# Kernel tuning notes

Hardware: AMD Instinct MI355X
Metric: run time of the kernel (lower is better)

Reference implementation:

```python
import jax, jax.numpy as jnp
import numpy as np

# AdaptiveLogSoftmaxWithLoss config (input_dim=2048, n_classes=50257, div_value=4.0)
CUTOFFS = [1000, 10000, 50257]  # torch appends n_classes
N_CLUSTERS = 2                   # len(CUTOFFS) - 1
HEAD_SIZE = CUTOFFS[0] + N_CLUSTERS  # 1002
D = 2048
HSZ = [D // 4, D // 16]          # tail hidden sizes: [512, 128]
N_TOK = 4096


def setup_inputs() -> dict:
    key = jax.random.key(0)
    ks = jax.random.split(key, 7)
    w = 0.02  # weight scale so logits stay O(1)
    x = jax.random.normal(ks[0], (N_TOK, D), dtype=jnp.float32)
    W_head = jax.random.normal(ks[1], (HEAD_SIZE, D), dtype=jnp.float32) * w
    W1_0 = jax.random.normal(ks[2], (HSZ[0], D), dtype=jnp.float32) * w
    W2_0 = jax.random.normal(ks[3], (CUTOFFS[1] - CUTOFFS[0], HSZ[0]), dtype=jnp.float32) * w  # [9000, 512]
    W1_1 = jax.random.normal(ks[4], (HSZ[1], D), dtype=jnp.float32) * w
    W2_1 = jax.random.normal(ks[5], (CUTOFFS[2] - CUTOFFS[1], HSZ[1]), dtype=jnp.float32) * w  # [40257, 128]
    target = jax.random.randint(ks[6], (N_TOK,), 0, CUTOFFS[2], dtype=jnp.int32)
    return {"x": x, "target": target, "W_head": W_head,
            "W1_0": W1_0, "W2_0": W2_0, "W1_1": W1_1, "W2_1": W2_1}


def reference(x, target, W_head, W1_0, W2_0, W1_1, W2_1):
    # head: [N, 1002] = [1000 frequent classes | 2 cluster logits]
    head = x @ W_head.T
    head_lsm = jax.nn.log_softmax(head, axis=-1)

    t = target
    # log-prob of target if it lies in the head (clip keeps gather in-range; masked later)
    head_lp = jnp.take_along_axis(head_lsm, jnp.clip(t, 0, CUTOFFS[0] - 1)[:, None], axis=1)[:, 0]

    def tail_target_lp(W1, W2, low, high, cluster_idx):
        # two-stage projection: [N,D] @ [D,h] @ [h,osz]
        logits = (x @ W1.T) @ W2.T                     # [N, high-low]
        lsm = jax.nn.log_softmax(logits, axis=-1)
        idx = jnp.clip(t - low, 0, high - low - 1)
        g = jnp.take_along_axis(lsm, idx[:, None], axis=1)[:, 0]
        # combine with head's cluster log-prob
        return head_lsm[:, CUTOFFS[0] + cluster_idx] + g

    lp0 = tail_target_lp(W1_0, W2_0, CUTOFFS[0], CUTOFFS[1], 0)
    lp1 = tail_target_lp(W1_1, W2_1, CUTOFFS[1], CUTOFFS[2], 1)

    out = jnp.where(t < CUTOFFS[0], head_lp, jnp.where(t < CUTOFFS[1], lp0, lp1))
    loss = -jnp.mean(out)
    return out, loss
```

## Files before the change

### kernel.cpp

```cpp
#include <hip/hip_runtime.h>
#include <hip/hip_bf16.h>
#include <math.h>

#define NTOK 4096
#define DIM 2048
#define NHEAD 1002
#define NCAT 1664
#define C0LO 1000
#define C0HI 10000
#define OSZ0 9000
#define OSZ1 40257
#define H0S 512
#define H1S 128
#define JS0 24
#define JS1 16
#define HEADBLKS 8
#define NT0 71
#define NT1 315

typedef __attribute__((ext_vector_type(4))) short short4v;
typedef __attribute__((ext_vector_type(8))) short short8v;
typedef __attribute__((ext_vector_type(4))) float f32x4;
typedef __hip_bfloat16 bf16;

#define GLOBAL_AS __attribute__((address_space(1)))
#define LDS_AS __attribute__((address_space(3)))

#define RAW_BAR() __builtin_amdgcn_s_barrier()
#define SCHED_FENCE() __builtin_amdgcn_sched_barrier(0)
#define WAIT_VM(N) asm volatile("s_waitcnt vmcnt(" #N ")" ::: "memory")
#define WAIT_LGKM0() asm volatile("s_waitcnt lgkmcnt(0)" ::: "memory")

__global__ __launch_bounds__(256) void cvt_all(
    const float* __restrict__ x, const float* __restrict__ W_head,
    const float* __restrict__ W1_0, const float* __restrict__ W1_1,
    const float* __restrict__ W2_0, const float* __restrict__ W2_1,
    bf16* __restrict__ xb, bf16* __restrict__ Wcat,
    bf16* __restrict__ W20b, bf16* __restrict__ W21b) {
  const long NX = (long)NTOK * DIM / 8;
  const long NC = (long)NCAT * DIM / 8;
  const long N20 = (long)OSZ0 * H0S / 8;
  const long N21 = (long)OSZ1 * H1S / 8;
  long gid = (long)blockIdx.x * 256 + threadIdx.x;
  const float* src = nullptr;
  bf16* dst;
  if (gid < NX) {
    src = x + gid * 8; dst = xb + gid * 8;
  } else if (gid < NX + NC) {
    long o = (gid - NX) * 8;
    int row = (int)(o >> 11), k = (int)(o & 2047);
    dst = Wcat + o;
    if (row < NHEAD) src = W_head + (long)row * DIM + k;
    else if (row < 1024) src = nullptr;
    else if (row < 1536) src = W1_0 + (long)(row - 1024) * DIM + k;
    else src = W1_1 + (long)(row - 1536) * DIM + k;
  } else if (gid < NX + NC + N20) {
    long o = (gid - NX - NC) * 8; src = W2_0 + o; dst = W20b + o;
  } else if (gid < NX + NC + N20 + N21) {
    long o = (gid - NX - NC - N20) * 8; src = W2_1 + o; dst = W21b + o;
  } else {
    return;
  }
  union { short8v v; bf16 h[8]; } u;
  if (src) {
    float4 a = *reinterpret_cast<const float4*>(src);
    float4 b = *reinterpret_cast<const float4*>(src + 4);
    u.h[0] = __float2bfloat16(a.x); u.h[1] = __float2bfloat16(a.y);
    u.h[2] = __float2bfloat16(a.z); u.h[3] = __float2bfloat16(a.w);
    u.h[4] = __float2bfloat16(b.x); u.h[5] = __float2bfloat16(b.y);
    u.h[6] = __float2bfloat16(b.z); u.h[7] = __float2bfloat16(b.w);
  } else {
#pragma unroll
    for (int e = 0; e < 8; ++e) u.h[e] = __float2bfloat16(0.f);
  }
  *reinterpret_cast<short8v*>(dst) = u.v;
}

__device__ __forceinline__ void stage_tile(const bf16* __restrict__ g, int row0,
                                           int maxrow, int ld, int k0,
                                           char* lds, int wave, int lane) {
#pragma unroll
  for (int c = 0; c < 4; ++c) {
    int rbase = wave * 32 + c * 8;
    int row = rbase + (lane >> 3);
    int grow = row0 + row;
    grow = grow < maxrow ? grow : maxrow;
    int slot = (lane & 7) ^ (row & 7);
    const bf16* src = g + (size_t)grow * ld + k0 + slot * 8;
    __builtin_amdgcn_global_load_lds((const GLOBAL_AS unsigned int*)src,
                                     (LDS_AS unsigned int*)(lds + rbase * 128),
                                     16, 0, 0);
  }
}

__device__ __forceinline__ short8v read_frag(const char* lds, int row, int kk, int lane) {
  int g = lane >> 4;
  int r7 = row & 7;
  int b1 = kk * 64 + g * 8;
  int b2 = b1 + 32;
  b1 = ((b1 >> 4) ^ r7) * 16 + (b1 & 15);
  b2 = ((b2 >> 4) ^ r7) * 16 + (b2 & 15);
  const char* p = lds + row * 128;
  short4v lo = *reinterpret_cast<const short4v*>(p + b1);
  short4v hi = *reinterpret_cast<const short4v*>(p + b2);
  return __builtin_shufflevector(lo, hi, 0, 1, 2, 3, 4, 5, 6, 7);
}

__device__ __forceinline__ void stage_tile256(const bf16* __restrict__ g, int row0,
                                              int maxrow, int ld,
                                              char* lds, int wave, int lane) {
#pragma unroll
  for (int c = 0; c < 8; ++c) {
    int rbase = wave * 32 + c * 4;
    int row = rbase + (lane >> 4);
    int grow = row0 + row;
    grow = grow < maxrow ? grow : maxrow;
    int slot = (lane & 15) ^ (row & 7);
    const bf16* src = g + (size_t)grow * ld + slot * 8;
    __builtin_amdgcn_global_load_lds((const GLOBAL_AS unsigned int*)src,
                                     (LDS_AS unsigned int*)(lds + rbase * 256),
                                     16, 0, 0);
  }
}

__device__ __forceinline__ short8v read_frag256(const char* lds, int row, int kk, int lane) {
  int g = lane >> 4;
  int r7 = row & 7;
  int b1 = kk * 64 + g * 8;
  int b2 = b1 + 32;
  b1 = (((b1 >> 4) ^ r7) << 4) | (b1 & 15);
  b2 = (((b2 >> 4) ^ r7) << 4) | (b2 & 15);
  const char* p = lds + row * 256;
  short4v lo = *reinterpret_cast<const short4v*>(p + b1);
  short4v hi = *reinterpret_cast<const short4v*>(p + b2);
  return __builtin_shufflevector(lo, hi, 0, 1, 2, 3, 4, 5, 6, 7);
}

__device__ __forceinline__ void reduce_write_ps(float srun[4][4], float* reds,
                                                float* ps, int slice, int tok0,
                                                int lane, int wr, int wc) {
#pragma unroll
  for (int off = 1; off < 16; off <<= 1)
#pragma unroll
    for (int m = 0; m < 4; ++m)
#pragma unroll
      for (int r = 0; r < 4; ++r) srun[m][r] += __shfl_xor(srun[m][r], off);
  __syncthreads();
  if (wc == 0 && (lane & 15) == 0) {
#pragma unroll
    for (int m = 0; m < 4; ++m)
#pragma unroll
      for (int r = 0; r < 4; ++r)
        reds[wr * 64 + m * 16 + (lane >> 4) * 4 + r] = srun[m][r];
  }
  __syncthreads();
  if (wc == 1 && (lane & 15) == 0) {
#pragma unroll
    for (int m = 0; m < 4; ++m)
#pragma unroll
      for (int r = 0; r < 4; ++r) {
        int row = wr * 64 + m * 16 + (lane >> 4) * 4 + r;
        ps[(size_t)slice * NTOK + tok0 + row] = reds[row] + srun[m][r];
      }
  }
}

__global__ __launch_bounds__(256, 3) void tail0_lse(
    const bf16* __restrict__ Ab, const bf16* __restrict__ W2b,
    float* __restrict__ ps) {
  __shared__ __align__(16) char As[128 * 128];
  __shared__ __align__(16) char Bs[128 * 128];
  __shared__ float reds[128];
  int tid = threadIdx.x;
  int lane = tid & 63, wave = tid >> 6;
  int wr = wave >> 1, wc = wave & 1;
  int wgid = blockIdx.x;
  int cx = wgid & 7, w = wgid >> 3;
  int tb = cx * 4 + (w & 3);
  int ys = w >> 2;
  int tok0 = tb * 128;
  int t_lo = (NT0 * ys) / JS0, t_hi = (NT0 * (ys + 1)) / JS0;
  float srun[4][4] = {};
  for (int jt = t_lo; jt < t_hi; ++jt) {
    int j0 = jt * 128;
    f32x4 acc[4][4] = {};
    for (int k0 = 0; k0 < H0S; k0 += 64) {
      __syncthreads();
      stage_tile(Ab, tok0, NTOK - 1, H0S, k0, As, wave, lane);
      stage_tile(W2b, j0, OSZ0 - 1, H0S, k0, Bs, wave, lane);
      __syncthreads();
#pragma unroll
      for (int kk = 0; kk < 2; ++kk) {
        short8v af[4], bfr[4];
#pragma unroll
        for (int m = 0; m < 4; ++m)
          af[m] = read_frag(As, wr * 64 + m * 16 + (lane & 15), kk, lane);
#pragma unroll
        for (int n = 0; n < 4; ++n)
          bfr[n] = read_frag(Bs, wc * 64 + n * 16 + (lane & 15), kk, lane);
#pragma unroll
        for (int m = 0; m < 4; ++m)
#pragma unroll
          for (int n = 0; n < 4; ++n)
            acc[m][n] = __builtin_amdgcn_mfma_f32_16x16x32_bf16(af[m], bfr[n], acc[m][n], 0, 0, 0);
      }
    }
#pragma unroll
    for (int m = 0; m < 4; ++m)
#pragma unroll
      for (int n = 0; n < 4; ++n) {
        int col = j0 + wc * 64 + n * 16 + (lane & 15);
        if (col < OSZ0) {
#pragma unroll
          for (int r = 0; r < 4; ++r) srun[m][r] += __expf(acc[m][n][r]);
        }
      }
  }
  reduce_write_ps(srun, reds, ps, ys, tok0, lane, wr, wc);
}

__device__ void tail1_body(const bf16* __restrict__ Ab, const bf16* __restrict__ W2b,
                           float* __restrict__ ps, char* lds) {
  char* buf0 = lds;
  char* buf1 = lds + 32768;
  float* reds = (float*)(lds + 65536);
  int tid = threadIdx.x;
  int lane = tid & 63, wave = tid >> 6;
  int wr = wave >> 1, wc = wave & 1;
  int wgid = blockIdx.x;
  int cx = wgid & 7, w = wgid >> 3;
  int tb = cx * 4 + (w & 3);
  int ys = w >> 2;
  int tok0 = tb * 128;
  int t_lo = (NT1 * ys) / JS1, t_hi = (NT1 * (ys + 1)) / JS1;
  int nt = t_hi - t_lo;

  stage_tile256(Ab, tok0, NTOK - 1, H1S, buf1, wave, lane);
  WAIT_VM(0); SCHED_FENCE();
  RAW_BAR();
  short8v afr[4][4];
#pragma unroll
  for (int kk = 0; kk < 4; ++kk)
#pragma unroll
    for (int m = 0; m < 4; ++m)
      afr[kk][m] = read_frag256(buf1, wr * 64 + m * 16 + (lane & 15), kk, lane);
  stage_tile256(W2b, t_lo * 128, OSZ1 - 1, H1S, buf0, wave, lane);
  WAIT_LGKM0(); SCHED_FENCE();
  RAW_BAR();
  if (nt > 1) stage_tile256(W2b, (t_lo + 1) * 128, OSZ1 - 1, H1S, buf1, wave, lane);

  float srun[4][4] = {};
  for (int i = 0; i < nt; ++i) {
    char* cur = (i & 1) ? buf1 : buf0;
    if (i + 1 < nt) { WAIT_VM(8); } else { WAIT_VM(0); }
    SCHED_FENCE();
    RAW_BAR();
    int j0 = (t_lo + i) * 128;
    f32x4 acc[4][4] = {};
#pragma unroll
    for (int kk = 0; kk < 4; ++kk) {
      short8v bfr[4];
#pragma unroll
      for (int n = 0; n < 4; ++n)
        bfr[n] = read_frag256(cur, wc * 64 + n * 16 + (lane & 15), kk, lane);
#pragma unroll
      for (int m = 0; m < 4; ++m)
#pragma unroll
        for (int n = 0; n < 4; ++n)
          acc[m][n] = __builtin_amdgcn_mfma_f32_16x16x32_bf16(afr[kk][m], bfr[n], acc[m][n], 0, 0, 0);
    }
#pragma unroll
    for (int m = 0; m < 4; ++m)
#pragma unroll
      for (int n = 0; n < 4; ++n) {
        int col = j0 + wc * 64 + n * 16 + (lane & 15);
        if (col < OSZ1) {
#pragma unroll
          for (int r = 0; r < 4; ++r) srun[m][r] += __expf(acc[m][n][r]);
        }
      }
    SCHED_FENCE();
    RAW_BAR();
    if (i + 2 < nt) stage_tile256(W2b, (t_lo + i + 2) * 128, OSZ1 - 1, H1S, cur, wave, lane);
  }
  reduce_write_ps(srun, reds, ps, ys, tok0, lane, wr, wc);
}

__global__ __launch_bounds__(256, 2) void tail1_lse(
    const bf16* __restrict__ Ab, const bf16* __restrict__ W2b,
    float* __restrict__ ps) {
  __shared__ __align__(16) char lds[66048];
  tail1_body(Ab, W2b, ps, lds);
}

__global__ __launch_bounds__(256, 3) void proj_gemm(
    const bf16* __restrict__ A, const bf16* __restrict__ B,
    float* __restrict__ head, float* __restrict__ h0, bf16* __restrict__ h0b,
    float* __restrict__ h1, bf16* __restrict__ h1b, float* __restrict__ ps_head) {
  __shared__ __align__(16) char As[16384];
  __shared__ __align__(16) char Bs[16384];
  __shared__ float reds[128];
  int tid = threadIdx.x;
  int lane = tid & 63, wave = tid >> 6;
  int wr = wave >> 1, wc = wave & 1;
  int wgid = blockIdx.x;
  int cx = wgid & 7, w = wgid >> 3;
  int col_b = w >> 2;
  int row_b = cx * 4 + (w & 3);
  int row0 = row_b * 128, col0 = col_b * 128;
  f32x4 acc[4][4] = {};
  for (int k0 = 0; k0 < DIM; k0 += 64) {
    __syncthreads();
    stage_tile(A, row0, NTOK - 1, DIM, k0, As, wave, lane);
    stage_tile(B, col0, NCAT - 1, DIM, k0, Bs, wave, lane);
    __syncthreads();
#pragma unroll
    for (int kk = 0; kk < 2; ++kk) {
      short8v af[4], bfr[4];
#pragma unroll
      for (int m = 0; m < 4; ++m)
        af[m] = read_frag(As, wr * 64 + m * 16 + (lane & 15), kk, lane);
#pragma unroll
      for (int n = 0; n < 4; ++n)
        bfr[n] = read_frag(Bs, wc * 64 + n * 16 + (lane & 15), kk, lane);
#pragma unroll
      for (int m = 0; m < 4; ++m)
#pragma unroll
        for (int n = 0; n < 4; ++n)
          acc[m][n] = __builtin_amdgcn_mfma_f32_16x16x32_bf16(af[m], bfr[n], acc[m][n], 0, 0, 0);
    }
  }
  float srun[4][4] = {};
#pragma unroll
  for (int m = 0; m < 4; ++m) {
    int row = row0 + wr * 64 + m * 16 + (lane >> 4) * 4;
#pragma unroll
    for (int n = 0; n < 4; ++n) {
      int col = col0 + wc * 64 + n * 16 + (lane & 15);
#pragma unroll
      for (int r = 0; r < 4; ++r) {
        float v = acc[m][n][r];
        if (col < NHEAD) {
          head[(size_t)(row + r) * NHEAD + col] = v;
          srun[m][r] += __expf(v);
        } else if (col >= 1024 && col < 1536) {
          h0[(size_t)(row + r) * H0S + (col - 1024)] = v;
          h0b[(size_t)(row + r) * H0S + (col - 1024)] = __float2bfloat16(v);
        } else if (col >= 1536) {
          h1[(size_t)(row + r) * H1S + (col - 1536)] = v;
          h1b[(size_t)(row + r) * H1S + (col - 1536)] = __float2bfloat16(v);
        }
      }
    }
  }
  if (col_b < HEADBLKS) {
    reduce_write_ps(srun, reds, ps_head, col_b, row0, lane, wr, wc);
  }
}

__global__ __launch_bounds__(256) void finalize2(
    const int* __restrict__ target, const float* __restrict__ head,
    const float* __restrict__ ps_head,
    const float* __restrict__ h0, const float* __restrict__ h1,
    const float* __restrict__ W2_0, const float* __restrict__ W2_1,
    const float* __restrict__ ps0, const float* __restrict__ ps1,
    float* __restrict__ out) {
  int warp = threadIdx.x >> 6, lane = threadIdx.x & 63;
  int i = blockIdx.x * 4 + warp;
  if (i >= NTOK) return;
  int t = target[i];
  float sh = 0.f;
#pragma unroll
  for (int s = 0; s < HEADBLKS; ++s) sh += ps_head[(size_t)s * NTOK + i];
  float lse_head = logf(sh);
  float res;
  if (t < C0LO) {
    res = head[(size_t)i * NHEAD + t] - lse_head;
  } else {
    int c = (t < C0HI) ? 0 : 1;
    int H = c ? H1S : H0S;
    int low = c ? C0HI : C0LO;
    const float* hv = (c ? h1 : h0) + (size_t)i * H;
    const float* wv = (c ? W2_1 : W2_0) + (size_t)(t - low) * H;
    float p = 0.f;
    for (int k = lane * 4; k < H; k += 256) {
      float4 a = *reinterpret_cast<const float4*>(hv + k);
      float4 b = *reinterpret_cast<const float4*>(wv + k);
      p += a.x * b.x + a.y * b.y + a.z * b.z + a.w * b.w;
    }
#pragma unroll
    for (int off = 32; off > 0; off >>= 1) p += __shfl_xor(p, off);
    const float* ps = c ? ps1 : ps0;
    int js = c ? JS1 : JS0;
    float S = 0.f;
    for (int s = 0; s < js; ++s) S += ps[(size_t)s * NTOK + i];
    float cl = head[(size_t)i * NHEAD + C0LO + c];
    res = (cl - lse_head) + (p - logf(S));
  }
  if (lane == 0) out[i] = res;
}

__global__ __launch_bounds__(256) void loss_kernel(float* __restrict__ out) {
  __shared__ float red[256];
  int tid = threadIdx.x;
  float s = 0.f;
  for (int j = tid; j < NTOK; j += 256) s += out[j];
  red[tid] = s; __syncthreads();
  for (int off = 128; off > 0; off >>= 1) {
    if (tid < off) red[tid] += red[tid + off];
    __syncthreads();
  }
  if (tid == 0) out[NTOK] = -red[0] / (float)NTOK;
}

extern "C" void kernel_launch(void* const* d_in, const int* in_sizes, int n_in,
                              void* d_out, int out_size, void* d_ws, size_t ws_size,
                              hipStream_t stream) {
  (void)in_sizes; (void)n_in; (void)out_size; (void)ws_size;
  const float* x = (const float*)d_in[0];
  const int* target = (const int*)d_in[1];
  const float* W_head = (const float*)d_in[2];
  const float* W1_0 = (const float*)d_in[3];
  const float* W2_0 = (const float*)d_in[4];
  const float* W1_1 = (const float*)d_in[5];
  const float* W2_1 = (const float*)d_in[6];
  float* out = (float*)d_out;

  char* w = (char*)d_ws;
  size_t off = 0;
  auto alloc = [&](size_t bytes) -> void* {
    void* p = w + off;
    off = (off + bytes + 255) & ~(size_t)255;
    return p;
  };
  bf16* xb   = (bf16*)alloc((size_t)NTOK * DIM * 2);
  bf16* Wcat = (bf16*)alloc((size_t)NCAT * DIM * 2);
  bf16* W20b = (bf16*)alloc((size_t)OSZ0 * H0S * 2);
  bf16* W21b = (bf16*)alloc((size_t)OSZ1 * H1S * 2);
  float* head = (float*)alloc((size_t)NTOK * NHEAD * 4);
  float* h0   = (float*)alloc((size_t)NTOK * H0S * 4);
  bf16*  h0b  = (bf16*)alloc((size_t)NTOK * H0S * 2);
  float* h1   = (float*)alloc((size_t)NTOK * H1S * 4);
  bf16*  h1b  = (bf16*)alloc((size_t)NTOK * H1S * 2);
  float* ps_head = (float*)alloc((size_t)HEADBLKS * NTOK * 4);
  float* ps0 = (float*)alloc((size_t)JS0 * NTOK * 4);
  float* ps1 = (float*)alloc((size_t)JS1 * NTOK * 4);

  dim3 blk(256);
  const long TOT8 = (long)NTOK * DIM / 8 + (long)NCAT * DIM / 8 +
                    (long)OSZ0 * H0S / 8 + (long)OSZ1 * H1S / 8;
  cvt_all<<<dim3((unsigned)((TOT8 + 255) / 256)), blk, 0, stream>>>(
      x, W_head, W1_0, W1_1, W2_0, W2_1, xb, Wcat, W20b, W21b);

  proj_gemm<<<dim3(416), blk, 0, stream>>>(
      xb, Wcat, head, h0, h0b, h1, h1b, ps_head);

  tail0_lse<<<dim3(32 * JS0), blk, 0, stream>>>(h0b, W20b, ps0);
  tail1_lse<<<dim3(32 * JS1), blk, 0, stream>>>(h1b, W21b, ps1);

  finalize2<<<dim3(NTOK / 4), blk, 0, stream>>>(target, head, ps_head, h0, h1,
                                                W2_0, W2_1, ps0, ps1, out);
  loss_kernel<<<1, blk, 0, stream>>>(out);
}
```

Measured before the change: 208.3 us.

## Pre-permute bf16 K layout so MFMA fragments load as single 16-byte LDS reads

The conversion kernel and the proj_gemm epilogue now write bf16 operands with the K dimension permuted in groups of 32. Each MFMA fragment therefore sits in one contiguous 16-byte chunk, and read_frag becomes a single 128-bit LDS load instead of two 64-bit loads plus a shuffle. Because the permutation is applied to both operands, the dot products are unchanged. The tail kernels also switch from a swizzled 1D block-index mapping to a plain 2D grid, which drops the earlier L2-locality block ordering.

```diff
diff --git a/kernel.cpp b/kernel.cpp
--- a/kernel.cpp
+++ b/kernel.cpp
@@ -31,6 +31,10 @@
 #define WAIT_VM(N) asm volatile("s_waitcnt vmcnt(" #N ")" ::: "memory")
 #define WAIT_LGKM0() asm volatile("s_waitcnt lgkmcnt(0)" ::: "memory")
 
+__device__ __forceinline__ int kperm(int c) {
+  return (c & ~31) | (((c & 15) >> 2) << 3) | (((c >> 4) & 1) << 2) | (c & 3);
+}
+
 __global__ __launch_bounds__(256) void cvt_all(
     const float* __restrict__ x, const float* __restrict__ W_head,
     const float* __restrict__ W1_0, const float* __restrict__ W1_1,
@@ -42,29 +46,44 @@
   const long N20 = (long)OSZ0 * H0S / 8;
   const long N21 = (long)OSZ1 * H1S / 8;
   long gid = (long)blockIdx.x * 256 + threadIdx.x;
-  const float* src = nullptr;
+  const float* s1 = nullptr;
+  const float* s2 = nullptr;
   bf16* dst;
+  long rel;
   if (gid < NX) {
-    src = x + gid * 8; dst = xb + gid * 8;
+    rel = gid * 8;
+    long c1 = (rel & ~31L) + ((rel >> 3) & 3) * 4;
+    s1 = x + c1; s2 = x + c1 + 16;
+    dst = xb + rel;
   } else if (gid < NX + NC) {
-    long o = (gid - NX) * 8;
-    int row = (int)(o >> 11), k = (int)(o & 2047);
-    dst = Wcat + o;
-    if (row < NHEAD) src = W_head + (long)row * DIM + k;
-    else if (row < 1024) src = nullptr;
-    else if (row < 1536) src = W1_0 + (long)(row - 1024) * DIM + k;
-    else src = W1_1 + (long)(row - 1536) * DIM + k;
+    rel = (gid - NX) * 8;
+    int row = (int)(rel >> 11);
+    long c1 = (rel & ~31L) + ((rel >> 3) & 3) * 4;
+    int col = (int)(c1 & 2047);
+    dst = Wcat + rel;
+    const float* srow = nullptr;
+    if (row < NHEAD) srow = W_head + (long)row * DIM;
+    else if (row < 1024) srow = nullptr;
+    else if (row < 1536) srow = W1_0 + (long)(row - 1024) * DIM;
+    else srow = W1_1 + (long)(row - 1536) * DIM;
+    if (srow) { s1 = srow + col; s2 = srow + col + 16; }
   } else if (gid < NX + NC + N20) {
-    long o = (gid - NX - NC) * 8; src = W2_0 + o; dst = W20b + o;
+    rel = (gid - NX - NC) * 8;
+    long c1 = (rel & ~31L) + ((rel >> 3) & 3) * 4;
+    s1 = W2_0 + c1; s2 = W2_0 + c1 + 16;
+    dst = W20b + rel;
   } else if (gid < NX + NC + N20 + N21) {
-    long o = (gid - NX - NC - N20) * 8; src = W2_1 + o; dst = W21b + o;
+    rel = (gid - NX - NC - N20) * 8;
+    long c1 = (rel & ~31L) + ((rel >> 3) & 3) * 4;
+    s1 = W2_1 + c1; s2 = W2_1 + c1 + 16;
+    dst = W21b + rel;
   } else {
     return;
   }
   union { short8v v; bf16 h[8]; } u;
-  if (src) {
-    float4 a = *reinterpret_cast<const float4*>(src);
-    float4 b = *reinterpret_cast<const float4*>(src + 4);
+  if (s1) {
+    float4 a = *reinterpret_cast<const float4*>(s1);
+    float4 b = *reinterpret_cast<const float4*>(s2);
     u.h[0] = __float2bfloat16(a.x); u.h[1] = __float2bfloat16(a.y);
     u.h[2] = __float2bfloat16(a.z); u.h[3] = __float2bfloat16(a.w);
     u.h[4] = __float2bfloat16(b.x); u.h[5] = __float2bfloat16(b.y);
@@ -94,16 +113,8 @@
 }
 
 __device__ __forceinline__ short8v read_frag(const char* lds, int row, int kk, int lane) {
-  int g = lane >> 4;
-  int r7 = row & 7;
-  int b1 = kk * 64 + g * 8;
-  int b2 = b1 + 32;
-  b1 = ((b1 >> 4) ^ r7) * 16 + (b1 & 15);
-  b2 = ((b2 >> 4) ^ r7) * 16 + (b2 & 15);
-  const char* p = lds + row * 128;
-  short4v lo = *reinterpret_cast<const short4v*>(p + b1);
-  short4v hi = *reinterpret_cast<const short4v*>(p + b2);
-  return __builtin_shufflevector(lo, hi, 0, 1, 2, 3, 4, 5, 6, 7);
+  int slot = (kk * 4 + (lane >> 4)) ^ (row & 7);
+  return *reinterpret_cast<const short8v*>(lds + row * 128 + slot * 16);
 }
 
 __device__ __forceinline__ void stage_tile256(const bf16* __restrict__ g, int row0,
@@ -124,16 +135,8 @@
 }
 
 __device__ __forceinline__ short8v read_frag256(const char* lds, int row, int kk, int lane) {
-  int g = lane >> 4;
-  int r7 = row & 7;
-  int b1 = kk * 64 + g * 8;
-  int b2 = b1 + 32;
-  b1 = (((b1 >> 4) ^ r7) << 4) | (b1 & 15);
-  b2 = (((b2 >> 4) ^ r7) << 4) | (b2 & 15);
-  const char* p = lds + row * 256;
-  short4v lo = *reinterpret_cast<const short4v*>(p + b1);
-  short4v hi = *reinterpret_cast<const short4v*>(p + b2);
-  return __builtin_shufflevector(lo, hi, 0, 1, 2, 3, 4, 5, 6, 7);
+  int slot = (kk * 4 + (lane >> 4)) ^ (row & 7);
+  return *reinterpret_cast<const short8v*>(lds + row * 256 + slot * 16);
 }
 
 __device__ __forceinline__ void reduce_write_ps(float srun[4][4], float* reds,
@@ -174,11 +177,8 @@
   int tid = threadIdx.x;
   int lane = tid & 63, wave = tid >> 6;
   int wr = wave >> 1, wc = wave & 1;
-  int wgid = blockIdx.x;
-  int cx = wgid & 7, w = wgid >> 3;
-  int tb = cx * 4 + (w & 3);
-  int ys = w >> 2;
-  int tok0 = tb * 128;
+  int tok0 = blockIdx.x * 128;
+  int ys = blockIdx.y;
   int t_lo = (NT0 * ys) / JS0, t_hi = (NT0 * (ys + 1)) / JS0;
   float srun[4][4] = {};
   for (int jt = t_lo; jt < t_hi; ++jt) {
@@ -227,11 +227,8 @@
   int tid = threadIdx.x;
   int lane = tid & 63, wave = tid >> 6;
   int wr = wave >> 1, wc = wave & 1;
-  int wgid = blockIdx.x;
-  int cx = wgid & 7, w = wgid >> 3;
-  int tb = cx * 4 + (w & 3);
-  int ys = w >> 2;
-  int tok0 = tb * 128;
+  int tok0 = blockIdx.x * 128;
+  int ys = blockIdx.y;
   int t_lo = (NT1 * ys) / JS1, t_hi = (NT1 * (ys + 1)) / JS1;
   int nt = t_hi - t_lo;
 
@@ -344,11 +341,13 @@
           head[(size_t)(row + r) * NHEAD + col] = v;
           srun[m][r] += __expf(v);
         } else if (col >= 1024 && col < 1536) {
-          h0[(size_t)(row + r) * H0S + (col - 1024)] = v;
-          h0b[(size_t)(row + r) * H0S + (col - 1024)] = __float2bfloat16(v);
+          int c = col - 1024;
+          h0[(size_t)(row + r) * H0S + c] = v;
+          h0b[(size_t)(row + r) * H0S + kperm(c)] = __float2bfloat16(v);
         } else if (col >= 1536) {
-          h1[(size_t)(row + r) * H1S + (col - 1536)] = v;
-          h1b[(size_t)(row + r) * H1S + (col - 1536)] = __float2bfloat16(v);
+          int c = col - 1536;
+          h1[(size_t)(row + r) * H1S + c] = v;
+          h1b[(size_t)(row + r) * H1S + kperm(c)] = __float2bfloat16(v);
         }
       }
     }
@@ -455,8 +454,8 @@
   proj_gemm<<<dim3(416), blk, 0, stream>>>(
       xb, Wcat, head, h0, h0b, h1, h1b, ps_head);
 
-  tail0_lse<<<dim3(32 * JS0), blk, 0, stream>>>(h0b, W20b, ps0);
-  tail1_lse<<<dim3(32 * JS1), blk, 0, stream>>>(h1b, W21b, ps1);
+  tail0_lse<<<dim3(NTOK / 128, JS0), blk, 0, stream>>>(h0b, W20b, ps0);
+  tail1_lse<<<dim3(NTOK / 128, JS1), blk, 0, stream>>>(h1b, W21b, ps1);
 
   finalize2<<<dim3(NTOK / 4), blk, 0, stream>>>(target, head, ps_head, h0, h1,
                                                 W2_0, W2_1, ps0, ps1, out);
```

New measurement: 184.5 us. 1.13x faster.
